# Performance work log

Hardware: AMD Instinct MI355X
Metric: run time of the kernel (lower is better)

## Reference

```python
import jax, jax.numpy as jnp
import numpy as np

B, T, D, H, MLP, WIN = 4, 2048, 768, 12, 3072, 256
HD = D // H


def setup_inputs() -> dict:
    key = jax.random.key(0)
    ks = jax.random.split(key, 9)
    s = 0.02
    return {
        "x": jax.random.normal(ks[0], (B, T, D), jnp.float32),
        "in_proj_w": jax.random.normal(ks[1], (3 * D, D), jnp.float32) * s,
        "in_proj_b": jax.random.normal(ks[2], (3 * D,), jnp.float32) * s,
        "out_w": jax.random.normal(ks[3], (D, D), jnp.float32) * s,
        "out_b": jax.random.normal(ks[4], (D,), jnp.float32) * s,
        "w1": jax.random.normal(ks[5], (MLP, D), jnp.float32) * s,
        "b1": jax.random.normal(ks[6], (MLP,), jnp.float32) * s,
        "w2": jax.random.normal(ks[7], (D, MLP), jnp.float32) * s,
        "b2": jax.random.normal(ks[8], (D,), jnp.float32) * s,
        "ln1_g": jnp.ones((D,), jnp.float32),
        "ln1_b": jnp.zeros((D,), jnp.float32),
        "ln2_g": jnp.ones((D,), jnp.float32),
        "ln2_b": jnp.zeros((D,), jnp.float32),
        "window_size": WIN,
    }


def _layernorm(v, g, b, eps=1e-5):
    m = v.mean(-1, keepdims=True)
    var = ((v - m) ** 2).mean(-1, keepdims=True)
    return (v - m) / jnp.sqrt(var + eps) * g + b


def reference(x, in_proj_w, in_proj_b, out_w, out_b, w1, b1, w2, b2,
              ln1_g, ln1_b, ln2_g, ln2_b, window_size):
    Bx, Tx, Dx = x.shape
    # --- local (banded) multi-head self-attention on norm1(x) ---
    xn = _layernorm(x, ln1_g, ln1_b)
    qkv = xn @ in_proj_w.T + in_proj_b            # [B,T,3D]
    q, k, v = jnp.split(qkv, 3, axis=-1)
    to_heads = lambda t: t.reshape(Bx, Tx, H, HD).transpose(0, 2, 1, 3)  # [B,H,T,hd]
    q, k, v = to_heads(q), to_heads(k), to_heads(v)
    scale = jnp.asarray(1.0 / np.sqrt(HD), x.dtype)
    scores = jnp.einsum('bhqd,bhkd->bhqk', q, k) * scale  # [B,H,T,T]
    idx = jnp.arange(Tx)
    banned = jnp.abs(idx[:, None] - idx[None, :]) > window_size  # True = masked
    scores = jnp.where(banned, -jnp.inf, scores)
    attn = jax.nn.softmax(scores, axis=-1)
    o = jnp.einsum('bhqk,bhkd->bhqd', attn, v)
    o = o.transpose(0, 2, 1, 3).reshape(Bx, Tx, Dx)
    o = o @ out_w.T + out_b
    x = x + o
    # --- MLP block on norm2(x) ---
    xn = _layernorm(x, ln2_g, ln2_b)
    h = jax.nn.gelu(xn @ w1.T + b1, approximate=False)
    x = x + (h @ w2.T + b2)
    return x
```

## Files before the change

### kernel.cpp

```cpp
#include <hip/hip_runtime.h>
#include <hip/hip_bf16.h>

typedef __bf16 bf16;
typedef __bf16 v8bf __attribute__((ext_vector_type(8)));
typedef __bf16 v4bf __attribute__((ext_vector_type(4)));
typedef float  v4f  __attribute__((ext_vector_type(4)));

#define DEVI __device__ __forceinline__

constexpr int Bc   = 4;
constexpr int Tc   = 2048;
constexpr int Dc   = 768;
constexpr int Hc   = 12;
constexpr int HDc  = 64;
constexpr int MLPc = 3072;
constexpr int QKVc = 2304;
constexpr int BTc  = Bc * Tc;

DEVI float b2f(bf16 x) { return (float)x; }
DEVI bf16  f2b(float x) { return (bf16)x; }

#define GLDS(gp, lp) __builtin_amdgcn_global_load_lds( \
    (const __attribute__((address_space(1))) void*)(gp), \
    (__attribute__((address_space(3))) void*)(lp), 16, 0, 0)

__global__ __launch_bounds__(256) void cvt2_kernel(
    const float* __restrict__ s0, bf16* __restrict__ d0, int n0,
    const float* __restrict__ s1, bf16* __restrict__ d1)
{
    int i = blockIdx.x * 256 + threadIdx.x;
    const float* s; bf16* d; int j;
    if (i < n0) { s = s0; d = d0; j = i; }
    else        { s = s1; d = d1; j = i - n0; }
    float4 v = ((const float4*)s)[j];
    v4bf o = { f2b(v.x), f2b(v.y), f2b(v.z), f2b(v.w) };
    ((v4bf*)d)[j] = o;
}

__global__ __launch_bounds__(256) void ln_kernel(
    const float* __restrict__ x, const float* __restrict__ g,
    const float* __restrict__ bt, bf16* __restrict__ out)
{
    const int row = blockIdx.x;
    const int t = threadIdx.x;
    const float* xr = x + (size_t)row * Dc;
    float v[3];
    v[0] = xr[t];
    v[1] = xr[t + 256];
    v[2] = xr[t + 512];
    float s = v[0] + v[1] + v[2];
    float s2 = v[0]*v[0] + v[1]*v[1] + v[2]*v[2];
    #pragma unroll
    for (int off = 32; off > 0; off >>= 1) {
        s  += __shfl_down(s, off);
        s2 += __shfl_down(s2, off);
    }
    __shared__ float red[8];
    const int wave = t >> 6, lane = t & 63;
    if (lane == 0) { red[wave] = s; red[4 + wave] = s2; }
    __syncthreads();
    s  = red[0] + red[1] + red[2] + red[3];
    s2 = red[4] + red[5] + red[6] + red[7];
    const float mean = s * (1.0f / Dc);
    const float var  = s2 * (1.0f / Dc) - mean * mean;
    const float rstd = rsqrtf(var + 1e-5f);
    bf16* orow = out + (size_t)row * Dc;
    #pragma unroll
    for (int i = 0; i < 3; i++) {
        int c = t + i * 256;
        orow[c] = f2b((v[i] - mean) * rstd * g[c] + bt[c]);
    }
}

enum { EPI_QKV = 0, EPI_GELU_BF16 = 1, EPI_RESID_F32 = 2, EPI_ACC_F32 = 3 };

template <int EPI, int TN, int BK>
__global__ __launch_bounds__(256) void gemm_bt(
    const bf16* __restrict__ A, const bf16* __restrict__ Bw,
    const float* __restrict__ bias,
    bf16* __restrict__ Cb, float* __restrict__ Cf,
    const float* __restrict__ resf,
    int M, int N, int K, int lda, int ldb)
{
    constexpr int MI = (TN == 128) ? 4 : 2;
    constexpr int CH = BK / 8;
    __shared__ __align__(16) bf16 sA[128 * BK];
    __shared__ __align__(16) bf16 sB[TN * BK];
    const int t = threadIdx.x, wave = t >> 6, lane = t & 63;
    const int moff = (TN == 128) ? (wave & 1) * 64 : wave * 32;
    const int noff = (TN == 128) ? (wave >> 1) * 64 : 0;
    const int nx = gridDim.x, ny = gridDim.y;
    const int nym = ny >> 3;
    const int bid = blockIdx.y * nx + blockIdx.x;
    const int xcd = bid & 7, kk = bid >> 3;
    const int m0 = (xcd * nym + kk % nym) * 128;
    const int n0 = (kk / nym) * TN;
    const bf16* Ag = A + (size_t)m0 * lda;
    const bf16* Bg = Bw + (size_t)n0 * ldb;

    v4f acc[MI][4];
    #pragma unroll
    for (int i = 0; i < MI; i++)
        #pragma unroll
        for (int j = 0; j < 4; j++) acc[i][j] = (v4f)(0.0f);

    for (int k0 = 0; k0 < K; k0 += BK) {
        #pragma unroll
        for (int i = 0; i < (128 * CH) / 256; i++) {
            int c = i * 256 + t;
            int r = c / CH, l0 = c % CH;
            int j = ((l0 & 7) ^ (r & 7)) | (l0 & ~7);
            GLDS(Ag + (size_t)r * lda + k0 + j * 8,
                 &sA[(i * 256 + wave * 64) * 8]);
        }
        #pragma unroll
        for (int i = 0; i < (TN * CH) / 256; i++) {
            int c = i * 256 + t;
            int r = c / CH, l0 = c % CH;
            int j = ((l0 & 7) ^ (r & 7)) | (l0 & ~7);
            GLDS(Bg + (size_t)r * ldb + k0 + j * 8,
                 &sB[(i * 256 + wave * 64) * 8]);
        }
        __syncthreads();
        #pragma unroll
        for (int ks = 0; ks < BK / 32; ks++) {
            const int rq = lane >> 4, rl = lane & 15;
            const int q = ks * 4 + rq;
            v8bf a[MI], b[4];
            #pragma unroll
            for (int mi = 0; mi < MI; mi++) {
                const int row = moff + mi * 16 + rl;
                const int l = ((q & 7) ^ (row & 7)) | (q & ~7);
                a[mi] = *(const v8bf*)&sA[row * BK + l * 8];
            }
            #pragma unroll
            for (int ni = 0; ni < 4; ni++) {
                const int row = noff + ni * 16 + rl;
                const int l = ((q & 7) ^ (row & 7)) | (q & ~7);
                b[ni] = *(const v8bf*)&sB[row * BK + l * 8];
            }
            #pragma unroll
            for (int mi = 0; mi < MI; mi++)
                #pragma unroll
                for (int ni = 0; ni < 4; ni++)
                    acc[mi][ni] = __builtin_amdgcn_mfma_f32_16x16x32_bf16(
                        a[mi], b[ni], acc[mi][ni], 0, 0, 0);
        }
        __syncthreads();
    }

    const int rq = lane >> 4, cn = lane & 15;
    #pragma unroll
    for (int mi = 0; mi < MI; mi++)
        #pragma unroll
        for (int ni = 0; ni < 4; ni++) {
            const int col = n0 + noff + ni * 16 + cn;
            const float bv = bias ? bias[col] : 0.0f;
            if constexpr (EPI == EPI_QKV) {
                const int row0 = m0 + moff + mi * 16 + rq * 4;
                if (n0 < 2 * Dc) {
                    bf16* dst = Cb + (col < Dc ? 0 : (size_t)BTc * Dc);
                    const int cadj = col < Dc ? col : col - Dc;
                    const float qs = (col < Dc) ? 0.18033688011112042f : 1.0f;
                    #pragma unroll
                    for (int r = 0; r < 4; r++)
                        dst[(size_t)(row0 + r) * Dc + cadj] = f2b((acc[mi][ni][r] + bv) * qs);
                } else {
                    const int vcol = col - 2 * Dc;
                    const int hh = vcol >> 6, hd = vcol & 63;
                    const int bb = row0 >> 11, t0 = row0 & 2047;
                    v4bf pk;
                    #pragma unroll
                    for (int r = 0; r < 4; r++) pk[r] = f2b(acc[mi][ni][r] + bv);
                    *(v4bf*)(Cb + 2 * (size_t)BTc * Dc +
                             (((size_t)bb * Hc + hh) * HDc + hd) * Tc + t0) = pk;
                }
            } else {
                #pragma unroll
                for (int r = 0; r < 4; r++) {
                    const int row = m0 + moff + mi * 16 + rq * 4 + r;
                    const size_t idx = (size_t)row * N + col;
                    float vv = acc[mi][ni][r] + bv;
                    if constexpr (EPI == EPI_GELU_BF16) {
                        Cb[idx] = f2b(0.5f * vv * (1.0f + erff(vv * 0.70710678118f)));
                    } else if constexpr (EPI == EPI_RESID_F32) {
                        Cf[idx] = vv + resf[idx];
                    } else {
                        Cf[idx] = vv + Cf[idx];
                    }
                }
            }
        }
}

__global__ __launch_bounds__(256, 3) void attn_kernel(
    const bf16* __restrict__ Qb, const bf16* __restrict__ Kb,
    const bf16* __restrict__ Vt, bf16* __restrict__ o,
    const int* __restrict__ winp)
{
    const int bh = blockIdx.x, qt = blockIdx.y;
    const int b = bh / Hc, h = bh % Hc;
    const int q0 = qt * 128;
    const int win = *winp;
    const int t = threadIdx.x, wave = t >> 6, lane = t & 63;
    const int rq = lane >> 4, cn = lane & 15;
    const int qw0 = q0 + wave * 32;

    __shared__ __align__(16) bf16 sK[64 * 64];
    __shared__ __align__(16) bf16 sV[64 * 64];
    __shared__ __align__(16) bf16 sP[4][32 * 64];
    bf16* const sPw = &sP[wave][0];
    const int swz = (cn & 7) << 1;

    const bf16* qp  = Qb + ((size_t)b * Tc) * Dc + h * HDc;
    const bf16* kp  = Kb + ((size_t)b * Tc) * Dc + h * HDc;
    const bf16* vtp = Vt + (size_t)bh * HDc * Tc;

    v8bf qf[2][2];
    #pragma unroll
    for (int ks = 0; ks < 2; ks++)
        #pragma unroll
        for (int mi = 0; mi < 2; mi++)
            qf[ks][mi] = *(const v8bf*)(qp + (size_t)(qw0 + mi * 16 + cn) * Dc
                                        + ks * 32 + rq * 8);

    v4f acc_o[2][4];
    #pragma unroll
    for (int mi = 0; mi < 2; mi++)
        #pragma unroll
        for (int nh = 0; nh < 4; nh++) acc_o[mi][nh] = (v4f)(0.0f);
    float l_part[2] = {0.0f, 0.0f};

    const int wlo = max(0, qw0 - win), whi = min(Tc - 1, qw0 + 31 + win);
    const int klo = max(0, q0 - win) & ~63;
    const int khi = min(Tc - 1, q0 + 127 + win);

    for (int kb0 = klo; kb0 <= khi; kb0 += 64) {
        #pragma unroll
        for (int i = 0; i < 2; i++) {
            int c = i * 256 + t;
            int r = c >> 3, j = (c & 7) ^ (r & 7);
            GLDS(kp + (size_t)(kb0 + r) * Dc + j * 8,
                 &sK[(i * 256 + wave * 64) * 8]);
            GLDS(vtp + (size_t)r * Tc + kb0 + j * 8,
                 &sV[(i * 256 + wave * 64) * 8]);
        }
        __syncthreads();

        if (kb0 + 63 >= wlo && kb0 <= whi) {
            v4f sf[4][2];
            #pragma unroll
            for (int kb = 0; kb < 4; kb++)
                #pragma unroll
                for (int mi = 0; mi < 2; mi++) sf[kb][mi] = (v4f)(0.0f);
            #pragma unroll
            for (int ks = 0; ks < 2; ks++) {
                v8bf kf[4];
                #pragma unroll
                for (int kb = 0; kb < 4; kb++) {
                    const int row = kb * 16 + cn;
                    kf[kb] = *(const v8bf*)&sK[row * 64
                                              + ((ks * 4 + rq) ^ (row & 7)) * 8];
                }
                #pragma unroll
                for (int kb = 0; kb < 4; kb++)
                    #pragma unroll
                    for (int mi = 0; mi < 2; mi++)
                        sf[kb][mi] = __builtin_amdgcn_mfma_f32_16x16x32_bf16(
                            kf[kb], qf[ks][mi], sf[kb][mi], 0, 0, 0);
            }

            const bool need_mask = (kb0 + 63 - qw0 > win) || (qw0 + 31 - kb0 > win);
            #pragma unroll
            for (int kb = 0; kb < 4; kb++)
                #pragma unroll
                for (int mi = 0; mi < 2; mi++) {
                    v4bf pk;
                    #pragma unroll
                    for (int r = 0; r < 4; r++) {
                        float tt = sf[kb][mi][r];
                        if (need_mask) {
                            int ki = kb0 + kb * 16 + rq * 4 + r;
                            int qi = qw0 + mi * 16 + cn;
                            int dd = qi - ki; dd = dd < 0 ? -dd : dd;
                            tt = (dd > win) ? -INFINITY : tt;
                        }
                        float p = exp2f(fminf(tt, 30.0f));
                        l_part[mi] += p;
                        pk[r] = f2b(p);
                    }
                    *(v4bf*)&sPw[(mi * 16 + cn) * 64
                                 + (((kb * 4 + rq) ^ swz) << 2)] = pk;
                }

            #pragma unroll
            for (int ks = 0; ks < 2; ks++) {
                v8bf pa[2], vf[4];
                #pragma unroll
                for (int mi = 0; mi < 2; mi++)
                    pa[mi] = *(const v8bf*)&sPw[(mi * 16 + cn) * 64
                                                + (((ks * 8 + rq * 2) ^ swz) << 2)];
                #pragma unroll
                for (int nh = 0; nh < 4; nh++) {
                    const int row = nh * 16 + cn;
                    vf[nh] = *(const v8bf*)&sV[row * 64
                                               + ((ks * 4 + rq) ^ (row & 7)) * 8];
                }
                #pragma unroll
                for (int mi = 0; mi < 2; mi++)
                    #pragma unroll
                    for (int nh = 0; nh < 4; nh++)
                        acc_o[mi][nh] = __builtin_amdgcn_mfma_f32_16x16x32_bf16(
                            pa[mi], vf[nh], acc_o[mi][nh], 0, 0, 0);
            }
        }
        __syncthreads();
    }

    #pragma unroll
    for (int mi = 0; mi < 2; mi++) {
        l_part[mi] += __shfl_xor(l_part[mi], 16);
        l_part[mi] += __shfl_xor(l_part[mi], 32);
    }

    bf16* ob = o + ((size_t)b * Tc + qw0) * Dc + h * HDc;
    #pragma unroll
    for (int mi = 0; mi < 2; mi++)
        #pragma unroll
        for (int r = 0; r < 4; r++) {
            const float lv = __shfl(l_part[mi], rq * 4 + r);
            const float invl = 1.0f / lv;
            #pragma unroll
            for (int nh = 0; nh < 4; nh++)
                ob[(size_t)(mi * 16 + rq * 4 + r) * Dc + nh * 16 + cn] =
                    f2b(acc_o[mi][nh][r] * invl);
        }
}

extern "C" void kernel_launch(void* const* d_in, const int* in_sizes, int n_in,
                              void* d_out, int out_size, void* d_ws, size_t ws_size,
                              hipStream_t stream)
{
    const float* x     = (const float*)d_in[0];
    const float* inw   = (const float*)d_in[1];
    const float* inb   = (const float*)d_in[2];
    const float* outw  = (const float*)d_in[3];
    const float* outb  = (const float*)d_in[4];
    const float* w1    = (const float*)d_in[5];
    const float* b1    = (const float*)d_in[6];
    const float* w2    = (const float*)d_in[7];
    const float* b2    = (const float*)d_in[8];
    const float* ln1g  = (const float*)d_in[9];
    const float* ln1b  = (const float*)d_in[10];
    const float* ln2g  = (const float*)d_in[11];
    const float* ln2b  = (const float*)d_in[12];
    const int*   winp  = (const int*)d_in[13];
    float* out = (float*)d_out;

    char* ws = (char*)d_ws;
    constexpr size_t A_OFF   = 0;
    constexpr size_t QKV_OFF = (size_t)BTc * Dc * 2;
    constexpr size_t WA_OFF  = QKV_OFF + 3 * (size_t)BTc * Dc * 2;
    constexpr size_t WS_NEED = WA_OFF + (size_t)(QKVc + Dc) * Dc * 2;
    if (ws_size < WS_NEED) return;

    bf16*  xn     = (bf16*)(ws + A_OFF);
    bf16*  qkvb   = (bf16*)(ws + QKV_OFF);
    bf16*  Qb     = qkvb;
    bf16*  Kb     = qkvb + (size_t)BTc * Dc;
    bf16*  Vt     = qkvb + 2 * (size_t)BTc * Dc;
    bf16*  hbuf   = (bf16*)(ws + QKV_OFF);
    bf16*  wmlp   = (bf16*)(ws + QKV_OFF + (size_t)BTc * (2 * Dc) * 2);
    bf16*  w1_b   = wmlp;
    bf16*  w2_b   = wmlp + (size_t)MLPc * Dc;
    bf16*  wqkv_b = (bf16*)(ws + WA_OFF);
    bf16*  wout_b = wqkv_b + (size_t)QKVc * Dc;

    constexpr int HALF = MLPc / 2;
    constexpr int NQKV4 = QKVc * Dc / 4, NOUT4 = Dc * Dc / 4;
    constexpr int NW14  = MLPc * Dc / 4, NW24  = Dc * MLPc / 4;

    cvt2_kernel<<<(NQKV4 + NOUT4) / 256, 256, 0, stream>>>(
        inw, wqkv_b, NQKV4, outw, wout_b);

    ln_kernel<<<BTc, 256, 0, stream>>>(x, ln1g, ln1b, xn);
    gemm_bt<EPI_QKV, 128, 64><<<dim3(QKVc / 128, BTc / 128), 256, 0, stream>>>(
        xn, wqkv_b, inb, qkvb, nullptr, nullptr, BTc, QKVc, Dc, Dc, Dc);
    attn_kernel<<<dim3(Bc * Hc, Tc / 128), 256, 0, stream>>>(Qb, Kb, Vt, xn, winp);
    cvt2_kernel<<<(NW14 + NW24) / 256, 256, 0, stream>>>(
        w1, w1_b, NW14, w2, w2_b);
    gemm_bt<EPI_RESID_F32, 64, 128><<<dim3(Dc / 64, BTc / 128), 256, 0, stream>>>(
        xn, wout_b, outb, nullptr, out, x, BTc, Dc, Dc, Dc, Dc);
    ln_kernel<<<BTc, 256, 0, stream>>>(out, ln2g, ln2b, xn);

    for (int c = 0; c < 2; c++) {
        const bf16* w1c = w1_b + (size_t)c * HALF * Dc;
        const bf16* w2c = w2_b + (size_t)c * HALF;
        gemm_bt<EPI_GELU_BF16, 128, 64><<<dim3(HALF / 128, BTc / 128), 256, 0, stream>>>(
            xn, w1c, b1 + c * HALF, hbuf, nullptr, nullptr, BTc, HALF, Dc, Dc, Dc);
        gemm_bt<EPI_ACC_F32, 64, 128><<<dim3(Dc / 64, BTc / 128), 256, 0, stream>>>(
            hbuf, w2c, (c == 0) ? b2 : nullptr, nullptr, out, nullptr,
            BTc, Dc, HALF, HALF, MLPc);
    }
}
```

Before: 369.9 us.

## Fuse weight conversion into layernorm, widen QKV tile, use MFMA for softmax row sums

```diff
diff --git a/kernel.cpp b/kernel.cpp
--- a/kernel.cpp
+++ b/kernel.cpp
@@ -24,26 +24,25 @@
     (const __attribute__((address_space(1))) void*)(gp), \
     (__attribute__((address_space(3))) void*)(lp), 16, 0, 0)
 
-__global__ __launch_bounds__(256) void cvt2_kernel(
-    const float* __restrict__ s0, bf16* __restrict__ d0, int n0,
-    const float* __restrict__ s1, bf16* __restrict__ d1)
-{
-    int i = blockIdx.x * 256 + threadIdx.x;
-    const float* s; bf16* d; int j;
-    if (i < n0) { s = s0; d = d0; j = i; }
-    else        { s = s1; d = d1; j = i - n0; }
-    float4 v = ((const float4*)s)[j];
-    v4bf o = { f2b(v.x), f2b(v.y), f2b(v.z), f2b(v.w) };
-    ((v4bf*)d)[j] = o;
-}
-
 __global__ __launch_bounds__(256) void ln_kernel(
     const float* __restrict__ x, const float* __restrict__ g,
-    const float* __restrict__ bt, bf16* __restrict__ out)
+    const float* __restrict__ bt, bf16* __restrict__ out,
+    const float* __restrict__ cs0, bf16* __restrict__ cd0, int n0c,
+    const float* __restrict__ cs1, bf16* __restrict__ cd1)
 {
-    const int row = blockIdx.x;
+    const int blk = blockIdx.x;
     const int t = threadIdx.x;
-    const float* xr = x + (size_t)row * Dc;
+    if (blk >= BTc) {
+        int i = (blk - BTc) * 256 + t;
+        const float* s; bf16* d; int j;
+        if (i < n0c) { s = cs0; d = cd0; j = i; }
+        else         { s = cs1; d = cd1; j = i - n0c; }
+        float4 v = ((const float4*)s)[j];
+        v4bf o = { f2b(v.x), f2b(v.y), f2b(v.z), f2b(v.w) };
+        ((v4bf*)d)[j] = o;
+        return;
+    }
+    const float* xr = x + (size_t)blk * Dc;
     float v[3];
     v[0] = xr[t];
     v[1] = xr[t + 256];
@@ -64,7 +63,7 @@
     const float mean = s * (1.0f / Dc);
     const float var  = s2 * (1.0f / Dc) - mean * mean;
     const float rstd = rsqrtf(var + 1e-5f);
-    bf16* orow = out + (size_t)row * Dc;
+    bf16* orow = out + (size_t)blk * Dc;
     #pragma unroll
     for (int i = 0; i < 3; i++) {
         int c = t + i * 256;
@@ -75,20 +74,21 @@
 enum { EPI_QKV = 0, EPI_GELU_BF16 = 1, EPI_RESID_F32 = 2, EPI_ACC_F32 = 3 };
 
 template <int EPI, int TN, int BK>
-__global__ __launch_bounds__(256) void gemm_bt(
+__global__ __launch_bounds__(256, 3) void gemm_bt(
     const bf16* __restrict__ A, const bf16* __restrict__ Bw,
     const float* __restrict__ bias,
     bf16* __restrict__ Cb, float* __restrict__ Cf,
     const float* __restrict__ resf,
     int M, int N, int K, int lda, int ldb)
 {
-    constexpr int MI = (TN == 128) ? 4 : 2;
+    constexpr int MI = (TN == 64) ? 2 : 4;
+    constexpr int NI = (TN == 192) ? 6 : 4;
     constexpr int CH = BK / 8;
     __shared__ __align__(16) bf16 sA[128 * BK];
     __shared__ __align__(16) bf16 sB[TN * BK];
     const int t = threadIdx.x, wave = t >> 6, lane = t & 63;
-    const int moff = (TN == 128) ? (wave & 1) * 64 : wave * 32;
-    const int noff = (TN == 128) ? (wave >> 1) * 64 : 0;
+    const int moff = (TN == 64) ? wave * 32 : (wave & 1) * 64;
+    const int noff = (TN == 64) ? 0 : (wave >> 1) * (NI * 16);
     const int nx = gridDim.x, ny = gridDim.y;
     const int nym = ny >> 3;
     const int bid = blockIdx.y * nx + blockIdx.x;
@@ -98,11 +98,11 @@
     const bf16* Ag = A + (size_t)m0 * lda;
     const bf16* Bg = Bw + (size_t)n0 * ldb;
 
-    v4f acc[MI][4];
+    v4f acc[MI][NI];
     #pragma unroll
     for (int i = 0; i < MI; i++)
         #pragma unroll
-        for (int j = 0; j < 4; j++) acc[i][j] = (v4f)(0.0f);
+        for (int j = 0; j < NI; j++) acc[i][j] = (v4f)(0.0f);
 
     for (int k0 = 0; k0 < K; k0 += BK) {
         #pragma unroll
@@ -126,7 +126,7 @@
         for (int ks = 0; ks < BK / 32; ks++) {
             const int rq = lane >> 4, rl = lane & 15;
             const int q = ks * 4 + rq;
-            v8bf a[MI], b[4];
+            v8bf a[MI], b[NI];
             #pragma unroll
             for (int mi = 0; mi < MI; mi++) {
                 const int row = moff + mi * 16 + rl;
@@ -134,7 +134,7 @@
                 a[mi] = *(const v8bf*)&sA[row * BK + l * 8];
             }
             #pragma unroll
-            for (int ni = 0; ni < 4; ni++) {
+            for (int ni = 0; ni < NI; ni++) {
                 const int row = noff + ni * 16 + rl;
                 const int l = ((q & 7) ^ (row & 7)) | (q & ~7);
                 b[ni] = *(const v8bf*)&sB[row * BK + l * 8];
@@ -142,7 +142,7 @@
             #pragma unroll
             for (int mi = 0; mi < MI; mi++)
                 #pragma unroll
-                for (int ni = 0; ni < 4; ni++)
+                for (int ni = 0; ni < NI; ni++)
                     acc[mi][ni] = __builtin_amdgcn_mfma_f32_16x16x32_bf16(
                         a[mi], b[ni], acc[mi][ni], 0, 0, 0);
         }
@@ -153,12 +153,12 @@
     #pragma unroll
     for (int mi = 0; mi < MI; mi++)
         #pragma unroll
-        for (int ni = 0; ni < 4; ni++) {
+        for (int ni = 0; ni < NI; ni++) {
             const int col = n0 + noff + ni * 16 + cn;
             const float bv = bias ? bias[col] : 0.0f;
             if constexpr (EPI == EPI_QKV) {
                 const int row0 = m0 + moff + mi * 16 + rq * 4;
-                if (n0 < 2 * Dc) {
+                if (col < 2 * Dc) {
                     bf16* dst = Cb + (col < Dc ? 0 : (size_t)BTc * Dc);
                     const int cadj = col < Dc ? col : col - Dc;
                     const float qs = (col < Dc) ? 0.18033688011112042f : 1.0f;
@@ -224,12 +224,16 @@
             qf[ks][mi] = *(const v8bf*)(qp + (size_t)(qw0 + mi * 16 + cn) * Dc
                                         + ks * 32 + rq * 8);
 
-    v4f acc_o[2][4];
-    #pragma unroll
-    for (int mi = 0; mi < 2; mi++)
+    v4f acc_o[2][4], acc_l[2];
+    #pragma unroll
+    for (int mi = 0; mi < 2; mi++) {
+        acc_l[mi] = (v4f)(0.0f);
         #pragma unroll
         for (int nh = 0; nh < 4; nh++) acc_o[mi][nh] = (v4f)(0.0f);
-    float l_part[2] = {0.0f, 0.0f};
+    }
+    v8bf vones;
+    #pragma unroll
+    for (int j = 0; j < 8; j++) vones[j] = f2b(1.0f);
 
     const int wlo = max(0, qw0 - win), whi = min(Tc - 1, qw0 + 31 + win);
     const int klo = max(0, q0 - win) & ~63;
@@ -285,9 +289,7 @@
                             int dd = qi - ki; dd = dd < 0 ? -dd : dd;
                             tt = (dd > win) ? -INFINITY : tt;
                         }
-                        float p = exp2f(fminf(tt, 30.0f));
-                        l_part[mi] += p;
-                        pk[r] = f2b(p);
+                        pk[r] = f2b(exp2f(tt));
                     }
                     *(v4bf*)&sPw[(mi * 16 + cn) * 64
                                  + (((kb * 4 + rq) ^ swz) << 2)] = pk;
@@ -306,6 +308,10 @@
                     vf[nh] = *(const v8bf*)&sV[row * 64
                                                + ((ks * 4 + rq) ^ (row & 7)) * 8];
                 }
+                #pragma unroll
+                for (int mi = 0; mi < 2; mi++)
+                    acc_l[mi] = __builtin_amdgcn_mfma_f32_16x16x32_bf16(
+                        pa[mi], vones, acc_l[mi], 0, 0, 0);
                 #pragma unroll
                 for (int mi = 0; mi < 2; mi++)
                     #pragma unroll
@@ -317,19 +323,12 @@
         __syncthreads();
     }
 
-    #pragma unroll
-    for (int mi = 0; mi < 2; mi++) {
-        l_part[mi] += __shfl_xor(l_part[mi], 16);
-        l_part[mi] += __shfl_xor(l_part[mi], 32);
-    }
-
     bf16* ob = o + ((size_t)b * Tc + qw0) * Dc + h * HDc;
     #pragma unroll
     for (int mi = 0; mi < 2; mi++)
         #pragma unroll
         for (int r = 0; r < 4; r++) {
-            const float lv = __shfl(l_part[mi], rq * 4 + r);
-            const float invl = 1.0f / lv;
+            const float invl = 1.0f / acc_l[mi][r];
             #pragma unroll
             for (int nh = 0; nh < 4; nh++)
                 ob[(size_t)(mi * 16 + rq * 4 + r) * Dc + nh * 16 + cn] =
@@ -379,19 +378,18 @@
     constexpr int HALF = MLPc / 2;
     constexpr int NQKV4 = QKVc * Dc / 4, NOUT4 = Dc * Dc / 4;
     constexpr int NW14  = MLPc * Dc / 4, NW24  = Dc * MLPc / 4;
-
-    cvt2_kernel<<<(NQKV4 + NOUT4) / 256, 256, 0, stream>>>(
-        inw, wqkv_b, NQKV4, outw, wout_b);
-
-    ln_kernel<<<BTc, 256, 0, stream>>>(x, ln1g, ln1b, xn);
-    gemm_bt<EPI_QKV, 128, 64><<<dim3(QKVc / 128, BTc / 128), 256, 0, stream>>>(
+    constexpr int CVA_BLKS = (NQKV4 + NOUT4) / 256;
+    constexpr int CVB_BLKS = (NW14 + NW24) / 256;
+
+    ln_kernel<<<BTc + CVA_BLKS, 256, 0, stream>>>(
+        x, ln1g, ln1b, xn, inw, wqkv_b, NQKV4, outw, wout_b);
+    gemm_bt<EPI_QKV, 192, 64><<<dim3(QKVc / 192, BTc / 128), 256, 0, stream>>>(
         xn, wqkv_b, inb, qkvb, nullptr, nullptr, BTc, QKVc, Dc, Dc, Dc);
     attn_kernel<<<dim3(Bc * Hc, Tc / 128), 256, 0, stream>>>(Qb, Kb, Vt, xn, winp);
-    cvt2_kernel<<<(NW14 + NW24) / 256, 256, 0, stream>>>(
-        w1, w1_b, NW14, w2, w2_b);
     gemm_bt<EPI_RESID_F32, 64, 128><<<dim3(Dc / 64, BTc / 128), 256, 0, stream>>>(
         xn, wout_b, outb, nullptr, out, x, BTc, Dc, Dc, Dc, Dc);
-    ln_kernel<<<BTc, 256, 0, stream>>>(out, ln2g, ln2b, xn);
+    ln_kernel<<<BTc + CVB_BLKS, 256, 0, stream>>>(
+        out, ln2g, ln2b, xn, w1, w1_b, NW14, w2, w2_b);
 
     for (int c = 0; c < 2; c++) {
         const bf16* w1c = w1_b + (size_t)c * HALF * Dc;
```

New measurement: 354.2 us. 1.04x faster.
